# Kernel tuning notes

Hardware: AMD Instinct MI355X
Metric: run time of the kernel (lower is better)

Reference implementation:

```python
import jax, jax.numpy as jnp
import numpy as np

N = 100000   # nodes
E = 400000   # edges
P = 250000   # permutations (substructures)
L = 16       # lrp_length
D = 16       # lrp_out_dim
M = P * L    # perm-length rows of the sparse gather matrices


def setup_inputs() -> dict:
    key = jax.random.key(0)
    ks = jax.random.split(key, 16)
    return {
        "nfeat": jax.random.normal(ks[0], (N, D), dtype=jnp.float32),
        "efeat_idx": jax.random.randint(ks[1], (E,), 0, 4, dtype=jnp.int64),
        "n_row": jnp.arange(M, dtype=jnp.int64),
        "n_col": jax.random.randint(ks[2], (M,), 0, N, dtype=jnp.int64),
        "n_val": jax.random.uniform(ks[3], (M,), dtype=jnp.float32),
        "e_row": jnp.arange(M, dtype=jnp.int64),
        "e_col": jax.random.randint(ks[4], (M,), 0, E, dtype=jnp.int64),
        "e_val": jax.random.uniform(ks[5], (M,), dtype=jnp.float32),
        "p_row": jax.random.randint(ks[6], (P,), 0, N, dtype=jnp.int64),
        "p_col": jnp.arange(P, dtype=jnp.int64),
        "p_val": jax.random.uniform(ks[7], (P,), dtype=jnp.float32),
        "degs": jax.random.uniform(ks[8], (N,), dtype=jnp.float32) * 10.0,
        "weights": jax.random.normal(ks[9], (D, D, L), dtype=jnp.float32),
        "bias": jnp.zeros((1, D), dtype=jnp.float32),
        "W0": jax.random.normal(ks[10], (1, 2 * D), dtype=jnp.float32),
        "b0": jnp.zeros((2 * D,), dtype=jnp.float32),
        "W1": jax.random.normal(ks[11], (2 * D, D), dtype=jnp.float32),
        "b1": jnp.zeros((D,), dtype=jnp.float32),
        "bond_emb": jax.random.normal(ks[12], (4, D), dtype=jnp.float32),
    }


def _spmm(row, col, val, mat, m):
    # torch_sparse.spmm(index, value, m, n, mat): out[r] += val * mat[c]
    return jax.ops.segment_sum(val[:, None] * mat[col], row, num_segments=m)


def reference(nfeat, efeat_idx, n_row, n_col, n_val, e_row, e_col, e_val,
              p_row, p_col, p_val, degs, weights, bias, W0, b0, W1, b1, bond_emb):
    efeat = bond_emb[efeat_idx]                              # [E, D]
    x = _spmm(n_row, n_col, n_val, nfeat, M) \
        + _spmm(e_row, e_col, e_val, efeat, M)               # [M, D], M = P*L
    # transpose(0,1).view(D, -1, L).permute(1, 2, 0) -> [P, L, D]
    x = x.T.reshape(D, P, L).transpose(1, 2, 0)
    # einsum('dab,bca->dc'): d=P, a=L, b=D_in, c=D_out
    x = jax.nn.relu(jnp.einsum('pld,dcl->pc', x, weights) + bias)  # [P, D]
    pooled = _spmm(p_row, p_col, p_val, x, N)                # [N, D]
    # degree gate MLP: 1 -> 2D -> D
    fd = jax.nn.relu(degs[:, None] @ W0 + b0) @ W1 + b1      # [N, D]
    return pooled * fd
```

## Files before the change

### kernel.cpp

```cpp
#include <hip/hip_runtime.h>

#define NP 250000
#define NN 100000
#define NE 400000
#define LL 16
#define DD 16
#define MM (NP * LL)
#define NTILES (NP / 16)

typedef __bf16 bf16x8 __attribute__((ext_vector_type(8)));
typedef float f32x4 __attribute__((ext_vector_type(4)));

__device__ __forceinline__ float4 fma4(float a, float4 b, float4 c) {
    float4 r;
    r.x = fmaf(a, b.x, c.x);
    r.y = fmaf(a, b.y, c.y);
    r.z = fmaf(a, b.z, c.z);
    r.w = fmaf(a, b.w, c.w);
    return r;
}

__global__ __launch_bounds__(256) void init_kernel(
    const float* __restrict__ w,
    const float* __restrict__ nfeat,
    const float* __restrict__ bond_emb,
    const int* __restrict__ e_col,
    const int* __restrict__ efeat_idx,
    __bf16* __restrict__ wfrag,
    __bf16* __restrict__ nfeat_bf,
    __bf16* __restrict__ bond_bf,
    unsigned char* __restrict__ be2,
    float* __restrict__ out)
{
    int t = blockIdx.x * 256 + threadIdx.x;
    if (t < 4096) {
        int kb = t >> 9;
        int lane = (t >> 3) & 63;
        int j = t & 7;
        int quad = lane >> 4, c = lane & 15;
        int d = ((quad & 1) << 3) + j;
        int l = ((quad >> 1) << 3) + kb;
        wfrag[t] = (__bf16)w[d * 256 + c * 16 + l];
    }
    if (t < NN * DD) {
        nfeat_bf[t] = (__bf16)nfeat[t];
        out[t] = 0.f;
    }
    if (t < 64) bond_bf[t] = (__bf16)bond_emb[t];
    if (t < MM / 4) {
        int4 ec = *(const int4*)(e_col + t * 4);
        unsigned int b0 = (unsigned int)efeat_idx[ec.x] & 3u;
        unsigned int b1 = (unsigned int)efeat_idx[ec.y] & 3u;
        unsigned int b2 = (unsigned int)efeat_idx[ec.z] & 3u;
        unsigned int b3 = (unsigned int)efeat_idx[ec.w] & 3u;
        be2[t] = (unsigned char)(b0 | (b1 << 2) | (b2 << 4) | (b3 << 6));
    }
}

__global__ __launch_bounds__(64) void perm_kernel(
    const __bf16* __restrict__ nfeat_bf,
    const int* __restrict__ n_col,
    const float* __restrict__ n_val,
    const float* __restrict__ e_val,
    const unsigned char* __restrict__ be2,
    const int* __restrict__ p_row,
    const float* __restrict__ p_val,
    const __bf16* __restrict__ wfrag,
    const float* __restrict__ bias,
    const __bf16* __restrict__ bond_bf,
    float* __restrict__ out)
{
    const int lane = threadIdx.x;
    const int tile = blockIdx.x;
    const int quad = lane >> 4;
    const int col = lane & 15;
    const int half = quad & 1;
    const int lhalf = quad >> 1;

    const int pbase = tile * 16;
    const int mbase = (pbase + col) * LL + lhalf * 8;

    int4   nca = *(const int4*)(n_col + mbase);
    int4   ncb = *(const int4*)(n_col + mbase + 4);
    float4 nva = *(const float4*)(n_val + mbase);
    float4 nvb = *(const float4*)(n_val + mbase + 4);
    float4 eva = *(const float4*)(e_val + mbase);
    float4 evb = *(const float4*)(e_val + mbase + 4);
    unsigned int be16 = *(const unsigned short*)(be2 + (mbase >> 2));
    int4   pr  = *(const int4*)(p_row + pbase + quad * 4);
    float4 pvv = *(const float4*)(p_val + pbase + quad * 4);

    bf16x8 wf[8];
#pragma unroll
    for (int kb = 0; kb < 8; ++kb)
        wf[kb] = *(const bf16x8*)(wfrag + (kb * 64 + lane) * 8);
    const bf16x8 bq0 = *(const bf16x8*)(bond_bf + 0 * 16 + half * 8);
    const bf16x8 bq1 = *(const bf16x8*)(bond_bf + 1 * 16 + half * 8);
    const bf16x8 bq2 = *(const bf16x8*)(bond_bf + 2 * 16 + half * 8);
    const bf16x8 bq3 = *(const bf16x8*)(bond_bf + 3 * 16 + half * 8);
    const float bias_c = bias[col];

    int   ncs[8] = {nca.x, nca.y, nca.z, nca.w, ncb.x, ncb.y, ncb.z, ncb.w};
    float nvs[8] = {nva.x, nva.y, nva.z, nva.w, nvb.x, nvb.y, nvb.z, nvb.w};
    float evs[8] = {eva.x, eva.y, eva.z, eva.w, evb.x, evb.y, evb.z, evb.w};

    bf16x8 nfr[8];
#pragma unroll
    for (int kb = 0; kb < 8; ++kb)
        nfr[kb] = *(const bf16x8*)(nfeat_bf + ncs[kb] * DD + half * 8);

    f32x4 acc = {0.f, 0.f, 0.f, 0.f};
#pragma unroll
    for (int kb = 0; kb < 8; ++kb) {
        unsigned int b = (be16 >> (2 * kb)) & 3u;
        bf16x8 blo = (b & 1) ? bq1 : bq0;
        bf16x8 bhi = (b & 1) ? bq3 : bq2;
        bf16x8 bsel = (b & 2) ? bhi : blo;
        float nv = nvs[kb], ev = evs[kb];
        bf16x8 af;
#pragma unroll
        for (int j = 0; j < 8; ++j)
            af[j] = (__bf16)fmaf(nv, (float)nfr[kb][j], ev * (float)bsel[j]);
        acc = __builtin_amdgcn_mfma_f32_16x16x32_bf16(af, wf[kb], acc, 0, 0, 0);
    }

    int   prs[4] = {pr.x, pr.y, pr.z, pr.w};
    float pvs[4] = {pvv.x, pvv.y, pvv.z, pvv.w};
#pragma unroll
    for (int r = 0; r < 4; ++r) {
        float v = fmaxf(acc[r] + bias_c, 0.f) * pvs[r];
        unsafeAtomicAdd(out + (size_t)prs[r] * DD + col, v);
    }
}

__global__ __launch_bounds__(256) void gate_kernel(
    const float* __restrict__ degs,
    const float* __restrict__ W0,
    const float* __restrict__ b0,
    const float* __restrict__ W1,
    const float* __restrict__ b1,
    float* __restrict__ out)
{
    int n = blockIdx.x * 256 + threadIdx.x;
    if (n >= NN) return;
    float dg = degs[n];
    float4 a0 = ((const float4*)b1)[0];
    float4 a1 = ((const float4*)b1)[1];
    float4 a2 = ((const float4*)b1)[2];
    float4 a3 = ((const float4*)b1)[3];
#pragma unroll
    for (int j = 0; j < 32; ++j) {
        float h = fmaxf(fmaf(dg, W0[j], b0[j]), 0.f);
        const float4* w1r = (const float4*)(W1 + j * 16);
        a0 = fma4(h, w1r[0], a0);
        a1 = fma4(h, w1r[1], a1);
        a2 = fma4(h, w1r[2], a2);
        a3 = fma4(h, w1r[3], a3);
    }
    float4* o = (float4*)(out + (size_t)n * DD);
    float4 v0 = o[0], v1 = o[1], v2 = o[2], v3 = o[3];
    v0.x *= a0.x; v0.y *= a0.y; v0.z *= a0.z; v0.w *= a0.w;
    v1.x *= a1.x; v1.y *= a1.y; v1.z *= a1.z; v1.w *= a1.w;
    v2.x *= a2.x; v2.y *= a2.y; v2.z *= a2.z; v2.w *= a2.w;
    v3.x *= a3.x; v3.y *= a3.y; v3.z *= a3.z; v3.w *= a3.w;
    o[0] = v0; o[1] = v1; o[2] = v2; o[3] = v3;
}

extern "C" void kernel_launch(void* const* d_in, const int* in_sizes, int n_in,
                              void* d_out, int out_size, void* d_ws, size_t ws_size,
                              hipStream_t stream) {
    const float* nfeat     = (const float*)d_in[0];
    const int*   efeat_idx = (const int*)d_in[1];
    const int*   n_col     = (const int*)d_in[3];
    const float* n_val     = (const float*)d_in[4];
    const int*   e_col     = (const int*)d_in[6];
    const float* e_val     = (const float*)d_in[7];
    const int*   p_row     = (const int*)d_in[8];
    const float* p_val     = (const float*)d_in[10];
    const float* degs      = (const float*)d_in[11];
    const float* weights   = (const float*)d_in[12];
    const float* bias      = (const float*)d_in[13];
    const float* W0        = (const float*)d_in[14];
    const float* b0        = (const float*)d_in[15];
    const float* W1        = (const float*)d_in[16];
    const float* b1        = (const float*)d_in[17];
    const float* bond_emb  = (const float*)d_in[18];

    float* out = (float*)d_out;

    char* wsb = (char*)d_ws;
    __bf16*        wfrag    = (__bf16*)wsb;
    __bf16*        nfeat_bf = (__bf16*)(wsb + 8192);
    __bf16*        bond_bf  = (__bf16*)(wsb + 8192 + 3200000);
    unsigned char* be2      = (unsigned char*)(wsb + 8192 + 3200000 + 128);

    init_kernel<<<(NN * DD + 255) / 256, 256, 0, stream>>>(
        weights, nfeat, bond_emb, e_col, efeat_idx,
        wfrag, nfeat_bf, bond_bf, be2, out);

    perm_kernel<<<NTILES, 64, 0, stream>>>(
        nfeat_bf, n_col, n_val, e_val, be2, p_row, p_val,
        wfrag, bias, bond_bf, out);

    gate_kernel<<<(NN + 255) / 256, 256, 0, stream>>>(degs, W0, b0, W1, b1, out);
}
```

Measured before the change: 213.6 us.

## Fuse degree gate into init and apply per-row gate before atomics

The degree-gate MLP is now computed in the init kernel into a workspace buffer. The perm kernel reads that buffer and multiplies each contribution by the gate before its atomic add, which removes the separate gate pass over the output. The perm kernel also goes from 64-thread to 256-thread blocks, four tiles per block. In exchange, every contribution does an extra gather read of the gate values, and the fused path depends on the workspace being large enough, otherwise it falls back to the separate gate kernel.

```diff
diff --git a/kernel.cpp b/kernel.cpp
--- a/kernel.cpp
+++ b/kernel.cpp
@@ -26,10 +26,16 @@
     const float* __restrict__ bond_emb,
     const int* __restrict__ e_col,
     const int* __restrict__ efeat_idx,
+    const float* __restrict__ degs,
+    const float* __restrict__ W0,
+    const float* __restrict__ b0,
+    const float* __restrict__ W1,
+    const float* __restrict__ b1,
     __bf16* __restrict__ wfrag,
     __bf16* __restrict__ nfeat_bf,
     __bf16* __restrict__ bond_bf,
     unsigned char* __restrict__ be2,
+    float* __restrict__ fd,
     float* __restrict__ out)
 {
     int t = blockIdx.x * 256 + threadIdx.x;
@@ -49,15 +55,33 @@
     if (t < 64) bond_bf[t] = (__bf16)bond_emb[t];
     if (t < MM / 4) {
         int4 ec = *(const int4*)(e_col + t * 4);
-        unsigned int b0 = (unsigned int)efeat_idx[ec.x] & 3u;
-        unsigned int b1 = (unsigned int)efeat_idx[ec.y] & 3u;
-        unsigned int b2 = (unsigned int)efeat_idx[ec.z] & 3u;
-        unsigned int b3 = (unsigned int)efeat_idx[ec.w] & 3u;
-        be2[t] = (unsigned char)(b0 | (b1 << 2) | (b2 << 4) | (b3 << 6));
-    }
-}
-
-__global__ __launch_bounds__(64) void perm_kernel(
+        unsigned int c0 = (unsigned int)efeat_idx[ec.x] & 3u;
+        unsigned int c1 = (unsigned int)efeat_idx[ec.y] & 3u;
+        unsigned int c2 = (unsigned int)efeat_idx[ec.z] & 3u;
+        unsigned int c3 = (unsigned int)efeat_idx[ec.w] & 3u;
+        be2[t] = (unsigned char)(c0 | (c1 << 2) | (c2 << 4) | (c3 << 6));
+    }
+    if (fd != nullptr && t < NN) {
+        float dg = degs[t];
+        float4 a0 = ((const float4*)b1)[0];
+        float4 a1 = ((const float4*)b1)[1];
+        float4 a2 = ((const float4*)b1)[2];
+        float4 a3 = ((const float4*)b1)[3];
+#pragma unroll
+        for (int j2 = 0; j2 < 32; ++j2) {
+            float h = fmaxf(fmaf(dg, W0[j2], b0[j2]), 0.f);
+            const float4* w1r = (const float4*)(W1 + j2 * 16);
+            a0 = fma4(h, w1r[0], a0);
+            a1 = fma4(h, w1r[1], a1);
+            a2 = fma4(h, w1r[2], a2);
+            a3 = fma4(h, w1r[3], a3);
+        }
+        float4* o = (float4*)(fd + (size_t)t * DD);
+        o[0] = a0; o[1] = a1; o[2] = a2; o[3] = a3;
+    }
+}
+
+__global__ __launch_bounds__(256) void perm_kernel(
     const __bf16* __restrict__ nfeat_bf,
     const int* __restrict__ n_col,
     const float* __restrict__ n_val,
@@ -68,10 +92,13 @@
     const __bf16* __restrict__ wfrag,
     const float* __restrict__ bias,
     const __bf16* __restrict__ bond_bf,
+    const float* __restrict__ fd,
     float* __restrict__ out)
 {
-    const int lane = threadIdx.x;
-    const int tile = blockIdx.x;
+    const int wid = threadIdx.x >> 6;
+    const int lane = threadIdx.x & 63;
+    const int tile = blockIdx.x * 4 + wid;
+    if (tile >= NTILES) return;
     const int quad = lane >> 4;
     const int col = lane & 15;
     const int half = quad & 1;
@@ -90,6 +117,14 @@
     int4   pr  = *(const int4*)(p_row + pbase + quad * 4);
     float4 pvv = *(const float4*)(p_val + pbase + quad * 4);
 
+    int   prs[4] = {pr.x, pr.y, pr.z, pr.w};
+    float gv[4] = {1.f, 1.f, 1.f, 1.f};
+    if (fd != nullptr) {
+#pragma unroll
+        for (int r = 0; r < 4; ++r)
+            gv[r] = fd[(size_t)prs[r] * DD + col];
+    }
+
     bf16x8 wf[8];
 #pragma unroll
     for (int kb = 0; kb < 8; ++kb)
@@ -124,11 +159,10 @@
         acc = __builtin_amdgcn_mfma_f32_16x16x32_bf16(af, wf[kb], acc, 0, 0, 0);
     }
 
-    int   prs[4] = {pr.x, pr.y, pr.z, pr.w};
     float pvs[4] = {pvv.x, pvv.y, pvv.z, pvv.w};
 #pragma unroll
     for (int r = 0; r < 4; ++r) {
-        float v = fmaxf(acc[r] + bias_c, 0.f) * pvs[r];
+        float v = fmaxf(acc[r] + bias_c, 0.f) * pvs[r] * gv[r];
         unsafeAtomicAdd(out + (size_t)prs[r] * DD + col, v);
     }
 }
@@ -193,14 +227,19 @@
     __bf16*        nfeat_bf = (__bf16*)(wsb + 8192);
     __bf16*        bond_bf  = (__bf16*)(wsb + 8192 + 3200000);
     unsigned char* be2      = (unsigned char*)(wsb + 8192 + 3200000 + 128);
+    const size_t base_need  = 8192 + 3200000 + 128 + 1000000;
+    const bool   fuse_gate  = ws_size >= base_need + (size_t)NN * DD * 4;
+    float*         fd       = fuse_gate ? (float*)(wsb + base_need) : nullptr;
 
     init_kernel<<<(NN * DD + 255) / 256, 256, 0, stream>>>(
         weights, nfeat, bond_emb, e_col, efeat_idx,
-        wfrag, nfeat_bf, bond_bf, be2, out);
-
-    perm_kernel<<<NTILES, 64, 0, stream>>>(
+        degs, W0, b0, W1, b1,
+        wfrag, nfeat_bf, bond_bf, be2, fd, out);
+
+    perm_kernel<<<(NTILES + 3) / 4, 256, 0, stream>>>(
         nfeat_bf, n_col, n_val, e_val, be2, p_row, p_val,
-        wfrag, bias, bond_bf, out);
-
-    gate_kernel<<<(NN + 255) / 256, 256, 0, stream>>>(degs, W0, b0, W1, b1, out);
-}
+        wfrag, bias, bond_bf, fd, out);
+
+    if (!fuse_gate)
+        gate_kernel<<<(NN + 255) / 256, 256, 0, stream>>>(degs, W0, b0, W1, b1, out);
+}
```

Result: faster. 207.4 us (-2.9%).
